# Kernel tuning notes

Hardware: AMD Instinct MI355X
Metric: run time of the kernel (lower is better)

Reference implementation:

```python
import jax, jax.numpy as jnp
import numpy as np

B, S, D, H = 2, 2048, 2048, 16
HD = D // H  # 128


def _rope_tables(seq_len, head_dim, base=10000.0):
    inv_freq = 1.0 / (base ** (np.arange(0, head_dim, 2, dtype=np.float32) / head_dim))
    t = np.arange(seq_len, dtype=np.float32)
    freqs = np.outer(t, inv_freq)  # [S, HD/2]
    return jnp.asarray(np.cos(freqs)), jnp.asarray(np.sin(freqs))


def setup_inputs() -> dict:
    key = jax.random.key(0)
    ks = jax.random.split(key, 5)
    std = 0.02
    inp = {
        "x": jax.random.normal(ks[0], (B, S, D), jnp.float32),
        "wq": jax.random.normal(ks[1], (D, D), jnp.float32) * std,
        "bq": jnp.zeros((D,), jnp.float32),
        "wk": jax.random.normal(ks[2], (D, D), jnp.float32) * std,
        "bk": jnp.zeros((D,), jnp.float32),
        "wv": jax.random.normal(ks[3], (D, D), jnp.float32) * std,
        "bv": jnp.zeros((D,), jnp.float32),
        "wo": jax.random.normal(ks[4], (D, D), jnp.float32) * std,
        "bo": jnp.zeros((D,), jnp.float32),
    }
    cos, sin = _rope_tables(S, HD)
    inp["freqs_cos"], inp["freqs_sin"] = cos, sin
    return inp


def _apply_rope(t, cos, sin):
    # t: [B,S,H,HD]; cos/sin: [S,HD/2] -> broadcast [1,S,1,HD/2]
    tp = t.reshape(*t.shape[:-1], HD // 2, 2)
    t1, t2 = tp[..., 0], tp[..., 1]
    c = cos[None, :, None, :]
    s = sin[None, :, None, :]
    out = jnp.stack([t1 * c - t2 * s, t1 * s + t2 * c], axis=-1)
    return out.reshape(t.shape)


def reference(x, wq, bq, wk, bk, wv, bv, wo, bo, freqs_cos, freqs_sin):
    b, s, d = x.shape
    q = (x @ wq.T + bq).reshape(b, s, H, HD)
    k = (x @ wk.T + bk).reshape(b, s, H, HD)
    v = (x @ wv.T + bv).reshape(b, s, H, HD)
    q = _apply_rope(q, freqs_cos, freqs_sin)
    k = _apply_rope(k, freqs_cos, freqs_sin)
    # causal SDPA: scores [B,H,S,S]
    scale = 1.0 / jnp.sqrt(jnp.asarray(HD, x.dtype))
    scores = jnp.einsum("bqhd,bkhd->bhqk", q, k) * scale
    causal = jnp.tril(jnp.ones((s, s), bool))
    scores = jnp.where(causal[None, None], scores, jnp.asarray(-1e30, scores.dtype))
    attn = jax.nn.softmax(scores.astype(jnp.float32), axis=-1).astype(x.dtype)
    out = jnp.einsum("bhqk,bkhd->bqhd", attn, v).reshape(b, s, d)
    return out @ wo.T + bo
```

## Files before the change

### kernel.cpp

```cpp
#include <hip/hip_runtime.h>


typedef __attribute__((ext_vector_type(8))) short short8;
typedef __attribute__((ext_vector_type(4))) float f32x4;
typedef __attribute__((ext_vector_type(16))) float f32x16;
typedef __attribute__((ext_vector_type(2))) unsigned short u16x2;
typedef __attribute__((ext_vector_type(4))) unsigned short u16x4;
typedef __attribute__((ext_vector_type(8))) unsigned short u16x8;

constexpr int Bc = 2, Sc = 2048, Dc = 2048, Hc = 16, HDc = 128;
constexpr int Mc = Bc * Sc;
constexpr int Nc = Dc, Kc = Dc;
constexpr float QSCL = 0.08838834764831845f * 1.4426950408889634f;

__device__ __forceinline__ unsigned short f2bf(float f) {
    union { float f; unsigned u; } x; x.f = f;
    unsigned r = x.u + 0x7FFFu + ((x.u >> 16) & 1u);
    return (unsigned short)(r >> 16);
}
__device__ __forceinline__ float bf2f(unsigned short u) {
    union { float f; unsigned u; } x; x.u = (unsigned)u << 16; return x.f;
}

__device__ __forceinline__ void g2lds16(const void* g, void* l) {
    __builtin_amdgcn_global_load_lds(
        (const __attribute__((address_space(1))) void*)g,
        (__attribute__((address_space(3))) void*)l, 16, 0, 0);
}

__device__ __forceinline__ void cvt_body(const float* __restrict__ in,
                                         unsigned short* __restrict__ out, int i) {
    f32x4 a = *((const f32x4*)in + (size_t)i * 2);
    f32x4 b = *((const f32x4*)in + (size_t)i * 2 + 1);
    u16x8 o;
    o[0] = f2bf(a[0]); o[1] = f2bf(a[1]); o[2] = f2bf(a[2]); o[3] = f2bf(a[3]);
    o[4] = f2bf(b[0]); o[5] = f2bf(b[1]); o[6] = f2bf(b[2]); o[7] = f2bf(b[3]);
    *((u16x8*)out + i) = o;
}

__global__ __launch_bounds__(256) void cvt_f32_bf16(
    const float* __restrict__ in, unsigned short* __restrict__ out, int n8) {
    int i = blockIdx.x * 256 + threadIdx.x;
    if (i >= n8) return;
    cvt_body(in, out, i);
}

__global__ __launch_bounds__(256) void cvt_batch(
    const float* __restrict__ x,  unsigned short* __restrict__ xo,
    const float* __restrict__ w0, unsigned short* __restrict__ o0,
    const float* __restrict__ w1, unsigned short* __restrict__ o1,
    const float* __restrict__ w2, unsigned short* __restrict__ o2,
    const float* __restrict__ w3, unsigned short* __restrict__ o3) {
    const int which = blockIdx.y;
    const float* in; unsigned short* out; int n8;
    if (which == 0)      { in = x;  out = xo; n8 = (Mc * Dc) / 8; }
    else if (which == 1) { in = w0; out = o0; n8 = (Dc * Dc) / 8; }
    else if (which == 2) { in = w1; out = o1; n8 = (Dc * Dc) / 8; }
    else if (which == 3) { in = w2; out = o2; n8 = (Dc * Dc) / 8; }
    else                 { in = w3; out = o3; n8 = (Dc * Dc) / 8; }
    int i = blockIdx.x * 256 + threadIdx.x;
    if (i >= n8) return;
    cvt_body(in, out, i);
}

template <int MODE>
__global__ __launch_bounds__(256) void gemm_nt(
    const unsigned short* __restrict__ A, const unsigned short* __restrict__ W,
    const float* __restrict__ bias, const float* __restrict__ rc,
    const float* __restrict__ rs, void* __restrict__ outp) {
    __shared__ __align__(16) unsigned short As[128 * 64];
    __shared__ __align__(16) unsigned short Bs[128 * 64];
    const int tid = threadIdx.x;
    const int w = tid >> 6, l = tid & 63;
    const int wm = w >> 1, wn = w & 1;
    const int lrow = l & 15, lhi = l >> 4;
    const int m0 = blockIdx.y * 128, n0 = blockIdx.x * 128;

    f32x4 acc[4][4];
#pragma unroll
    for (int i = 0; i < 4; ++i)
#pragma unroll
        for (int j = 0; j < 4; ++j) acc[i][j] = (f32x4){0.f, 0.f, 0.f, 0.f};

    for (int k0 = 0; k0 < Kc; k0 += 64) {
        __syncthreads();
#pragma unroll
        for (int i = 0; i < 4; ++i) {
            int s = i * 256 + tid;
            int row = s >> 3, c = s & 7;
            int cg = (c ^ (row & 7)) * 8;
            g2lds16(A + (size_t)(m0 + row) * Kc + k0 + cg,
                    &As[(size_t)(i * 256 + (w << 6)) * 8]);
            g2lds16(W + (size_t)(n0 + row) * Kc + k0 + cg,
                    &Bs[(size_t)(i * 256 + (w << 6)) * 8]);
        }
        __syncthreads();
#pragma unroll
        for (int kk = 0; kk < 2; ++kk) {
            short8 af[4], bf[4];
#pragma unroll
            for (int i = 0; i < 4; ++i) {
                int ra = wm * 64 + i * 16 + lrow;
                af[i] = *(const short8*)&As[ra * 64 + (((kk * 4 + lhi) ^ (ra & 7)) << 3)];
                int rb = wn * 64 + i * 16 + lrow;
                bf[i] = *(const short8*)&Bs[rb * 64 + (((kk * 4 + lhi) ^ (rb & 7)) << 3)];
            }
#pragma unroll
            for (int i = 0; i < 4; ++i)
#pragma unroll
                for (int j = 0; j < 4; ++j)
                    acc[i][j] = __builtin_amdgcn_mfma_f32_16x16x32_bf16(
                        af[i], bf[j], acc[i][j], 0, 0, 0);
        }
    }

#pragma unroll
    for (int i = 0; i < 4; ++i) {
#pragma unroll
        for (int j = 0; j < 4; ++j) {
            int gm0 = m0 + wm * 64 + i * 16 + lhi * 4;
            int gn  = n0 + wn * 64 + j * 16 + lrow;
            float bv = bias[gn];
            if (MODE == 0 || MODE == 1) {
                unsigned short* o = (unsigned short*)outp;
                int fi = (gn & (HDc - 1)) >> 1;
#pragma unroll
                for (int r = 0; r < 4; ++r) {
                    int gm = gm0 + r;
                    float v = acc[i][j][r] + bv;
                    float p = __shfl_xor(v, 1);
                    int pos = gm & (Sc - 1);
                    float cz = rc[pos * (HDc / 2) + fi];
                    float sz = rs[pos * (HDc / 2) + fi];
                    float ov = (gn & 1) ? (p * sz + v * cz) : (v * cz - p * sz);
                    if (MODE == 0) ov *= QSCL;
                    o[(size_t)gm * Nc + gn] = f2bf(ov);
                }
            } else if (MODE == 2) {
                unsigned short* o = (unsigned short*)outp;
                int b = gm0 >> 11, sb = gm0 & (Sc - 1);
                u16x4 pk;
#pragma unroll
                for (int r = 0; r < 4; ++r) pk[r] = f2bf(acc[i][j][r] + bv);
                *(u16x4*)&o[((size_t)b * Dc + gn) * Sc + sb] = pk;
            } else {
                float* o = (float*)outp;
#pragma unroll
                for (int r = 0; r < 4; ++r)
                    o[(size_t)(gm0 + r) * Nc + gn] = acc[i][j][r] + bv;
            }
        }
    }
}

#define ATTN_STAGE(tt, kd, vd) {                                               \
    const unsigned short* Kt = Kbase + (size_t)(tt) * 64 * Dc;                 \
    const unsigned short* Vp = Vbase + (tt) * 64;                              \
    _Pragma("unroll")                                                          \
    for (int i_ = 0; i_ < 4; ++i_) {                                           \
        int p_ = i_ * 256 + tid;                                               \
        int rK = p_ >> 4, sK = p_ & 15;                                        \
        g2lds16(Kt + (size_t)rK * Dc + ((sK ^ (rK & 15)) << 3),                \
                (kd) + (i_ * 256 + (w << 6)) * 8);                             \
        int rV = p_ >> 3, sV = p_ & 7;                                         \
        g2lds16(Vp + (size_t)rV * Sc + ((sV ^ (rV & 7)) << 3),                 \
                (vd) + (i_ * 256 + (w << 6)) * 8);                             \
    } }

#define ATTN_PVSTEP(PC, HB, KS) {                                              \
    int X0, X1, Y0, Y1;                                                        \
    asm("v_cvt_pk_bf16_f32 %0, %1, %2" : "=v"(X0) : "v"(PC[HB+0]), "v"(PC[HB+1])); \
    asm("v_cvt_pk_bf16_f32 %0, %1, %2" : "=v"(X1) : "v"(PC[HB+2]), "v"(PC[HB+3])); \
    asm("v_cvt_pk_bf16_f32 %0, %1, %2" : "=v"(Y0) : "v"(PC[HB+4]), "v"(PC[HB+5])); \
    asm("v_cvt_pk_bf16_f32 %0, %1, %2" : "=v"(Y1) : "v"(PC[HB+6]), "v"(PC[HB+7])); \
    asm("v_permlane32_swap_b32 %0, %1" : "+v"(X0), "+v"(Y0));                  \
    asm("v_permlane32_swap_b32 %0, %1" : "+v"(X1), "+v"(Y1));                  \
    union { int i[4]; short8 s; } pf_;                                         \
    pf_.i[0] = X0; pf_.i[1] = X1; pf_.i[2] = Y0; pf_.i[3] = Y1;                \
    _Pragma("unroll")                                                          \
    for (int dc_ = 0; dc_ < 4; ++dc_) {                                        \
        int rr = 32 * dc_ + ql;                                                \
        short8 vf = *(const short8*)&Vbuf[rr * 64 + (((2*(KS)+Hh) ^ (rr & 7)) << 3)]; \
        accv[dc_] = __builtin_amdgcn_mfma_f32_32x32x16_bf16(vf, pf_.s, accv[dc_], 0, 0, 0); \
    } }

#define ATTN_TILE_BODY(Kbuf, Vbuf, kb0)                                        \
    {                                                                          \
        f32x16 a0 = (f32x16)(0.f), a1 = (f32x16)(0.f);                         \
        __builtin_amdgcn_s_setprio(1);                                         \
        _Pragma("unroll")                                                      \
        for (int dc = 0; dc < 8; ++dc) {                                       \
            int r0 = ql, r1 = 32 + ql, sl = dc * 2 + Hh;                       \
            short8 k0 = *(const short8*)&Kbuf[r0 * 128 + ((sl ^ (r0 & 15)) << 3)]; \
            short8 k1 = *(const short8*)&Kbuf[r1 * 128 + ((sl ^ (r1 & 15)) << 3)]; \
            a0 = __builtin_amdgcn_mfma_f32_32x32x16_bf16(k0, qf[dc], a0, 0, 0, 0); \
            a1 = __builtin_amdgcn_mfma_f32_32x32x16_bf16(k1, qf[dc], a1, 0, 0, 0); \
        }                                                                      \
        __builtin_amdgcn_s_setprio(0);                                         \
        if ((kb0) >= 2 * qt * 64) {                                            \
            _Pragma("unroll")                                                  \
            for (int r = 0; r < 16; ++r) {                                     \
                int kl = (r & 3) + 8 * (r >> 2) + 4 * Hh;                      \
                if ((kb0) + kl > qg)      a0[r] = -3.0e38f;                    \
                if ((kb0) + 32 + kl > qg) a1[r] = -3.0e38f;                    \
            }                                                                  \
        }                                                                      \
        float m8[8];                                                           \
        _Pragma("unroll")                                                      \
        for (int r = 0; r < 8; ++r)                                            \
            m8[r] = fmaxf(fmaxf(a0[r], a0[r + 8]), fmaxf(a1[r], a1[r + 8]));   \
        float m4a = fmaxf(m8[0], m8[1]), m4b = fmaxf(m8[2], m8[3]);            \
        float m4c = fmaxf(m8[4], m8[5]), m4d = fmaxf(m8[6], m8[7]);            \
        float pm = fmaxf(fmaxf(m4a, m4b), fmaxf(m4c, m4d));                    \
        pm = fmaxf(pm, __shfl_xor(pm, 32));                                    \
        if (!__all(pm - mrun <= 8.0f)) {                                       \
            float mnew = fmaxf(mrun, pm);                                      \
            float fs = exp2f(mrun - mnew);                                     \
            mrun = mnew;                                                       \
            lrun *= fs;                                                        \
            _Pragma("unroll")                                                  \
            for (int dc = 0; dc < 4; ++dc)                                     \
                _Pragma("unroll")                                              \
                for (int r = 0; r < 16; ++r) accv[dc][r] *= fs;                \
        }                                                                      \
        float p0[16], p1[16];                                                  \
        _Pragma("unroll")                                                      \
        for (int r = 0; r < 16; ++r) p0[r] = exp2f(a0[r] - mrun);              \
        _Pragma("unroll")                                                      \
        for (int r = 0; r < 16; ++r) p1[r] = exp2f(a1[r] - mrun);              \
        float s8[8];                                                           \
        _Pragma("unroll")                                                      \
        for (int r = 0; r < 8; ++r)                                            \
            s8[r] = (p0[r] + p0[r + 8]) + (p1[r] + p1[r + 8]);                 \
        float s4a = s8[0] + s8[1], s4b = s8[2] + s8[3];                        \
        float s4c = s8[4] + s8[5], s4d = s8[6] + s8[7];                        \
        float ps = (s4a + s4b) + (s4c + s4d);                                  \
        lrun += ps + __shfl_xor(ps, 32);                                       \
        __builtin_amdgcn_s_setprio(1);                                         \
        ATTN_PVSTEP(p0, 0, 0); ATTN_PVSTEP(p0, 8, 1);                          \
        ATTN_PVSTEP(p1, 0, 2); ATTN_PVSTEP(p1, 8, 3);                          \
        __builtin_amdgcn_s_setprio(0);                                         \
    }

__global__ __launch_bounds__(256, 2) void attn_part(
    const unsigned short* __restrict__ Q, const unsigned short* __restrict__ Kb,
    const unsigned short* __restrict__ Vt, unsigned short* __restrict__ O,
    unsigned short* __restrict__ pacc, float* __restrict__ pml) {
    __shared__ __align__(16) unsigned short Ks[2][64 * 128];
    __shared__ __align__(16) unsigned short Vs[2][128 * 64];
    const int tid = threadIdx.x;
    const int w = tid >> 6, l = tid & 63;
    const int ql = l & 31, Hh = l >> 5;
    const int bh = blockIdx.x;
    const int slot = blockIdx.y;
    int qt, part, np;
    if (slot < 16) { qt = 15 - (slot >> 1); part = slot & 1; np = 2; }
    else           { qt = 23 - slot;        part = 0;        np = 1; }
    const int nt   = 2 * qt + 2;
    const int tbeg = part ? (qt + 1) : 0;
    const int tend = (np == 2 && part == 0) ? (qt + 1) : nt;
    const int b = bh >> 4, h = bh & 15;

    const unsigned short* Kbase = Kb + ((size_t)b * Sc) * Dc + h * HDc;
    const unsigned short* Vbase = Vt + ((size_t)b * Dc + h * HDc) * Sc;

    const int qw0 = qt * 128 + w * 32;
    const int qg = qw0 + ql;

    short8 qf[8];
    {
        const unsigned short* qp = Q + ((size_t)(b * Sc + qg)) * Dc + h * HDc;
#pragma unroll
        for (int dc = 0; dc < 8; ++dc)
            qf[dc] = *(const short8*)(qp + dc * 16 + Hh * 8);
    }
    f32x16 accv[4];
#pragma unroll
    for (int i = 0; i < 4; ++i) accv[i] = (f32x16)(0.f);
    float mrun = -3.0e38f, lrun = 0.f;

    ATTN_STAGE(tbeg, Ks[0], Vs[0]);
    for (int t = tbeg; t < tend; ++t) {
        const int cur = (t - tbeg) & 1;
        if (t + 1 < tend) {
            ATTN_STAGE(t + 1, Ks[cur ^ 1], Vs[cur ^ 1]);
            asm volatile("s_waitcnt vmcnt(8)" ::: "memory");
        } else {
            asm volatile("s_waitcnt vmcnt(0)" ::: "memory");
        }
        __builtin_amdgcn_s_barrier();

        const unsigned short* Kbuf = Ks[cur];
        const unsigned short* Vbuf = Vs[cur];
        const int kb0 = t * 64;
        if (kb0 <= qw0 + 31) ATTN_TILE_BODY(Kbuf, Vbuf, kb0);
        __builtin_amdgcn_s_barrier();
    }

    if (np == 1) {
        float inv = 1.f / lrun;
        unsigned short* Op = O + ((size_t)(b * Sc + qg)) * Dc + h * HDc;
#pragma unroll
        for (int dc = 0; dc < 4; ++dc)
#pragma unroll
            for (int rg = 0; rg < 4; ++rg) {
                int d0 = 32 * dc + 8 * rg + 4 * Hh;
                u16x4 pk;
#pragma unroll
                for (int j = 0; j < 4; ++j) pk[j] = f2bf(accv[dc][rg * 4 + j] * inv);
                *(u16x4*)(Op + d0) = pk;
            }
    } else {
        const int jslot = ((bh << 3) + (qt - 8)) * 2 + part;
        unsigned short* pa = pacc + (size_t)jslot * (128 * 128) + (w * 32 + ql) * 128;
#pragma unroll
        for (int dc = 0; dc < 4; ++dc)
#pragma unroll
            for (int rg = 0; rg < 4; ++rg) {
                u16x4 pk;
#pragma unroll
                for (int j = 0; j < 4; ++j) pk[j] = f2bf(accv[dc][rg * 4 + j]);
                *(u16x4*)&pa[32 * dc + 8 * rg + 4 * Hh] = pk;
            }
        if (Hh == 0) {
            float* pm2 = pml + (size_t)jslot * 256 + (w * 32 + ql) * 2;
            pm2[0] = mrun; pm2[1] = lrun;
        }
    }
}

__global__ __launch_bounds__(256) void attn_combine(
    const unsigned short* __restrict__ pacc, const float* __restrict__ pml,
    unsigned short* __restrict__ O) {
    const int w = threadIdx.x >> 6, l = threadIdx.x & 63;
    const int idx = blockIdx.x * 4 + w;
    const int jp = idx >> 7, row = idx & 127;
    const int bh = jp >> 3, qt = (jp & 7) + 8;
    const int b = bh >> 4, h = bh & 15;
    const unsigned short* a0 = pacc + ((size_t)jp * 2) * (128 * 128) + row * 128;
    const unsigned short* a1 = a0 + 128 * 128;
    const float* ml0 = pml + ((size_t)jp * 2) * 256 + row * 2;
    const float* ml1 = ml0 + 256;
    float m0 = ml0[0], l0 = ml0[1], m1 = ml1[0], l1 = ml1[1];
    float M = fmaxf(m0, m1);
    float w0 = exp2f(m0 - M), w1 = exp2f(m1 - M);
    float inv = 1.f / (l0 * w0 + l1 * w1);
    int d = l * 2;
    u16x2 v0 = *(const u16x2*)&a0[d];
    u16x2 v1 = *(const u16x2*)&a1[d];
    u16x2 pk;
    pk[0] = f2bf((bf2f(v0[0]) * w0 + bf2f(v1[0]) * w1) * inv);
    pk[1] = f2bf((bf2f(v0[1]) * w0 + bf2f(v1[1]) * w1) * inv);
    int qrow = qt * 128 + row;
    *(u16x2*)(O + ((size_t)(b * Sc + qrow)) * Dc + h * HDc + d) = pk;
}

__global__ __launch_bounds__(256, 2) void attn_fwd5(
    const unsigned short* __restrict__ Q, const unsigned short* __restrict__ Kb,
    const unsigned short* __restrict__ Vt, unsigned short* __restrict__ O) {
    __shared__ __align__(16) unsigned short Ks[2][64 * 128];
    __shared__ __align__(16) unsigned short Vs[2][128 * 64];
    const int tid = threadIdx.x;
    const int w = tid >> 6, l = tid & 63;
    const int ql = l & 31, Hh = l >> 5;
    const int bh = blockIdx.x;
    const int y = blockIdx.y;
    const int qt = (y < 8) ? y : (23 - y);
    const int b = bh >> 4, h = bh & 15;

    const unsigned short* Kbase = Kb + ((size_t)b * Sc) * Dc + h * HDc;
    const unsigned short* Vbase = Vt + ((size_t)b * Dc + h * HDc) * Sc;

    const int qw0 = qt * 128 + w * 32;
    const int qg = qw0 + ql;

    short8 qf[8];
    {
        const unsigned short* qp = Q + ((size_t)(b * Sc + qg)) * Dc + h * HDc;
#pragma unroll
        for (int dc = 0; dc < 8; ++dc)
            qf[dc] = *(const short8*)(qp + dc * 16 + Hh * 8);
    }
    f32x16 accv[4];
#pragma unroll
    for (int i = 0; i < 4; ++i) accv[i] = (f32x16)(0.f);
    float mrun = -3.0e38f, lrun = 0.f;
    const int nt = 2 * qt + 2;

    ATTN_STAGE(0, Ks[0], Vs[0]);
    for (int t = 0; t < nt; ++t) {
        if (t + 1 < nt) {
            ATTN_STAGE(t + 1, Ks[(t + 1) & 1], Vs[(t + 1) & 1]);
            asm volatile("s_waitcnt vmcnt(8)" ::: "memory");
        } else {
            asm volatile("s_waitcnt vmcnt(0)" ::: "memory");
        }
        __builtin_amdgcn_s_barrier();

        const unsigned short* Kbuf = Ks[t & 1];
        const unsigned short* Vbuf = Vs[t & 1];
        const int kb0 = t * 64;
        if (kb0 <= qw0 + 31) ATTN_TILE_BODY(Kbuf, Vbuf, kb0);
        __builtin_amdgcn_s_barrier();
    }
    float inv = 1.f / lrun;
    unsigned short* Op = O + ((size_t)(b * Sc + qg)) * Dc + h * HDc;
#pragma unroll
    for (int dc = 0; dc < 4; ++dc)
#pragma unroll
        for (int rg = 0; rg < 4; ++rg) {
            int d0 = 32 * dc + 8 * rg + 4 * Hh;
            u16x4 pk;
#pragma unroll
            for (int j = 0; j < 4; ++j) pk[j] = f2bf(accv[dc][rg * 4 + j] * inv);
            *(u16x4*)(Op + d0) = pk;
        }
}

extern "C" void kernel_launch(void* const* d_in, const int* in_sizes, int n_in,
                              void* d_out, int out_size, void* d_ws, size_t ws_size,
                              hipStream_t stream) {
    const float* x  = (const float*)d_in[0];
    const float* wq = (const float*)d_in[1];
    const float* bq = (const float*)d_in[2];
    const float* wk = (const float*)d_in[3];
    const float* bk = (const float*)d_in[4];
    const float* wv = (const float*)d_in[5];
    const float* bv = (const float*)d_in[6];
    const float* wo = (const float*)d_in[7];
    const float* bo = (const float*)d_in[8];
    const float* rc = (const float*)d_in[9];
    const float* rs = (const float*)d_in[10];

    const size_t NE = (size_t)Mc * Dc;
    const size_t NW = (size_t)Dc * Dc;

    unsigned short* xb = (unsigned short*)d_ws;
    unsigned short* qb = xb + NE;
    unsigned short* kb = qb + NE;
    unsigned short* vt = kb + NE;
    unsigned short* wb = vt + NE;

    const int ne8 = (int)(NE / 8), nw8 = (int)(NW / 8);
    dim3 gg(Nc / 128, Mc / 128), tb(256);
    const bool big_ws = ws_size >= (4 * NE + 4 * NW) * sizeof(unsigned short);

    if (big_ws) {
        unsigned short* wqb = wb;
        unsigned short* wkb = wb + NW;
        unsigned short* wvb = wb + 2 * NW;
        unsigned short* wob = wb + 3 * NW;
        unsigned short* pacc = wb;
        float* pml = (float*)(wb + 2 * NW);
        cvt_batch<<<dim3(ne8 / 256, 5), tb, 0, stream>>>(
            x, xb, wq, wqb, wk, wkb, wv, wvb, wo, wob);
        gemm_nt<0><<<gg, tb, 0, stream>>>(xb, wqb, bq, rc, rs, qb);
        gemm_nt<1><<<gg, tb, 0, stream>>>(xb, wkb, bk, rc, rs, kb);
        gemm_nt<2><<<gg, tb, 0, stream>>>(xb, wvb, bv, rc, rs, vt);
        attn_part<<<dim3(Bc * Hc, 24), tb, 0, stream>>>(qb, kb, vt, xb, pacc, pml);
        attn_combine<<<dim3(32 * 8 * 128 / 4), tb, 0, stream>>>(pacc, pml, xb);
        gemm_nt<3><<<gg, tb, 0, stream>>>(xb, wob, bo, rc, rs, d_out);
    } else {
        cvt_f32_bf16<<<dim3(ne8 / 256), tb, 0, stream>>>(x, xb, ne8);
        cvt_f32_bf16<<<dim3(nw8 / 256), tb, 0, stream>>>(wq, wb, nw8);
        gemm_nt<0><<<gg, tb, 0, stream>>>(xb, wb, bq, rc, rs, qb);
        cvt_f32_bf16<<<dim3(nw8 / 256), tb, 0, stream>>>(wk, wb, nw8);
        gemm_nt<1><<<gg, tb, 0, stream>>>(xb, wb, bk, rc, rs, kb);
        cvt_f32_bf16<<<dim3(nw8 / 256), tb, 0, stream>>>(wv, wb, nw8);
        gemm_nt<2><<<gg, tb, 0, stream>>>(xb, wb, bv, rc, rs, vt);
        attn_fwd5<<<dim3(Bc * Hc, 16), tb, 0, stream>>>(qb, kb, vt, xb);
        cvt_f32_bf16<<<dim3(nw8 / 256), tb, 0, stream>>>(wo, wb, nw8);
        gemm_nt<3><<<gg, tb, 0, stream>>>(xb, wb, bo, rc, rs, d_out);
    }
}
```

Measured before the change: 274.1 us.

## Fuse QKV projections into one triple-buffered 256x128 GEMM with 512 threads

Replaces the three separate Q/K/V GEMM launches with one gemm8 launch over the concatenated weight matrix (contiguous wq/wk/wv bf16 buffers), picking bias and epilogue (RoPE, transpose) per column block. The new kernel uses 256x128 tiles, 8 waves, a 3-stage LDS ring filled with global_load_lds, interleaved staging with MFMA, and setprio around MFMA bursts. The output projection also uses this kernel. It cuts launch count and improves overlap, at the cost of large LDS use (144KB per block) which limits occupancy.

```diff
diff --git a/kernel.cpp b/kernel.cpp
--- a/kernel.cpp
+++ b/kernel.cpp
@@ -11,6 +11,7 @@
 constexpr int Bc = 2, Sc = 2048, Dc = 2048, Hc = 16, HDc = 128;
 constexpr int Mc = Bc * Sc;
 constexpr int Nc = Dc, Kc = Dc;
+constexpr int NT = Kc / 64;
 constexpr float QSCL = 0.08838834764831845f * 1.4426950408889634f;
 
 __device__ __forceinline__ unsigned short f2bf(float f) {
@@ -61,6 +62,126 @@
     int i = blockIdx.x * 256 + threadIdx.x;
     if (i >= n8) return;
     cvt_body(in, out, i);
+}
+
+#define G8_STAGE_A(tt, rr, ii) {                                               \
+    int s_ = (ii) * 512 + tid, row_ = s_ >> 3, c_ = s_ & 7;                    \
+    g2lds16(A + (size_t)(m0 + row_) * Kc + (tt) * 64 + ((c_ ^ (row_ & 7)) << 3), \
+            &As[rr][(size_t)((ii) * 512 + (w << 6)) * 8]); }
+#define G8_STAGE_B(tt, rr, ii) {                                               \
+    int s_ = (ii) * 512 + tid, row_ = s_ >> 3, c_ = s_ & 7;                    \
+    g2lds16(W + (size_t)(n0 + row_) * Kc + (tt) * 64 + ((c_ ^ (row_ & 7)) << 3), \
+            &Bs[rr][(size_t)((ii) * 512 + (w << 6)) * 8]); }
+#define G8_RD_B(rr, kk) { _Pragma("unroll")                                    \
+    for (int j = 0; j < 4; ++j) {                                              \
+        int rb = wn * 64 + j * 16 + lrow;                                      \
+        bf[j] = *(const short8*)&Bs[rr][rb * 64 + ((((kk)*4 + lhi) ^ (rb & 7)) << 3)]; } }
+#define G8_RD_A(rr, kk, i0) {                                                  \
+    { int ra = wm * 64 + (i0) * 16 + lrow;                                     \
+      af0 = *(const short8*)&As[rr][ra * 64 + ((((kk)*4 + lhi) ^ (ra & 7)) << 3)]; } \
+    { int ra = wm * 64 + ((i0) + 1) * 16 + lrow;                               \
+      af1 = *(const short8*)&As[rr][ra * 64 + ((((kk)*4 + lhi) ^ (ra & 7)) << 3)]; } }
+#define G8_MFMA(i0) { _Pragma("unroll")                                        \
+    for (int j = 0; j < 4; ++j) {                                              \
+        acc[i0][j] = __builtin_amdgcn_mfma_f32_16x16x32_bf16(af0, bf[j], acc[i0][j], 0, 0, 0); \
+        acc[(i0)+1][j] = __builtin_amdgcn_mfma_f32_16x16x32_bf16(af1, bf[j], acc[(i0)+1][j], 0, 0, 0); } }
+#define G8_SYNC1 __builtin_amdgcn_s_barrier();                                 \
+    asm volatile("s_waitcnt lgkmcnt(0)" ::: "memory");                         \
+    __builtin_amdgcn_s_setprio(1);
+#define G8_SYNC2 __builtin_amdgcn_s_setprio(0); __builtin_amdgcn_s_barrier();
+
+template <int KIND>
+__global__ __launch_bounds__(512, 2) void gemm8(
+    const unsigned short* __restrict__ A, const unsigned short* __restrict__ W,
+    const float* __restrict__ bq, const float* __restrict__ bk,
+    const float* __restrict__ bv, const float* __restrict__ rc,
+    const float* __restrict__ rs, void* __restrict__ oq,
+    unsigned short* __restrict__ ok, unsigned short* __restrict__ ov) {
+    __shared__ __align__(16) unsigned short As[3][256 * 64];
+    __shared__ __align__(16) unsigned short Bs[3][128 * 64];
+    const int tid = threadIdx.x;
+    const int w = tid >> 6, l = tid & 63;
+    const int wm = w >> 1, wn = w & 1;
+    const int lrow = l & 15, lhi = l >> 4;
+    const int m0 = blockIdx.y * 256, n0 = blockIdx.x * 128;
+
+    f32x4 acc[4][4];
+#pragma unroll
+    for (int i = 0; i < 4; ++i)
+#pragma unroll
+        for (int j = 0; j < 4; ++j) acc[i][j] = (f32x4){0.f, 0.f, 0.f, 0.f};
+
+#pragma unroll
+    for (int ii = 0; ii < 4; ++ii) G8_STAGE_A(0, 0, ii);
+    G8_STAGE_B(0, 0, 0); G8_STAGE_B(0, 0, 1);
+#pragma unroll
+    for (int ii = 0; ii < 4; ++ii) G8_STAGE_A(1, 1, ii);
+    G8_STAGE_B(1, 1, 0); G8_STAGE_B(1, 1, 1);
+    asm volatile("s_waitcnt vmcnt(6)" ::: "memory");
+    __builtin_amdgcn_s_barrier();
+
+    short8 bf[4], af0, af1;
+    for (int t = 0; t < NT; ++t) {
+        const int r = t % 3, rn = (t + 2) % 3;
+        const bool st = (t + 2) < NT;
+        G8_RD_B(r, 0); G8_RD_A(r, 0, 0);
+        if (st) { G8_STAGE_A(t + 2, rn, 0); G8_STAGE_A(t + 2, rn, 1); }
+        G8_SYNC1; G8_MFMA(0); G8_SYNC2;
+        G8_RD_A(r, 0, 2);
+        if (st) { G8_STAGE_A(t + 2, rn, 2); G8_STAGE_A(t + 2, rn, 3); }
+        G8_SYNC1; G8_MFMA(2); G8_SYNC2;
+        G8_RD_B(r, 1); G8_RD_A(r, 1, 0);
+        if (st) G8_STAGE_B(t + 2, rn, 0);
+        G8_SYNC1; G8_MFMA(0); G8_SYNC2;
+        G8_RD_A(r, 1, 2);
+        if (st) {
+            G8_STAGE_B(t + 2, rn, 1);
+            asm volatile("s_waitcnt vmcnt(6)" ::: "memory");
+        } else {
+            asm volatile("s_waitcnt vmcnt(0)" ::: "memory");
+        }
+        G8_SYNC1; G8_MFMA(2); G8_SYNC2;
+    }
+
+    const int mode = (KIND == 1) ? 3 : (n0 >> 11);
+    const float* bias = (KIND == 1) ? bq : (mode == 0 ? bq : mode == 1 ? bk : bv);
+#pragma unroll
+    for (int i = 0; i < 4; ++i) {
+#pragma unroll
+        for (int j = 0; j < 4; ++j) {
+            int gm0 = m0 + wm * 64 + i * 16 + lhi * 4;
+            int gn  = n0 + wn * 64 + j * 16 + lrow;
+            int gnl = gn & (Dc - 1);
+            float bvv = bias[gnl];
+            if (mode == 0 || mode == 1) {
+                unsigned short* o = (unsigned short*)(mode == 0 ? oq : (void*)ok);
+                int fi = (gn & (HDc - 1)) >> 1;
+#pragma unroll
+                for (int rr = 0; rr < 4; ++rr) {
+                    int gm = gm0 + rr;
+                    float v = acc[i][j][rr] + bvv;
+                    float p = __shfl_xor(v, 1);
+                    int pos = gm & (Sc - 1);
+                    float cz = rc[pos * (HDc / 2) + fi];
+                    float sz = rs[pos * (HDc / 2) + fi];
+                    float ovv = (gn & 1) ? (p * sz + v * cz) : (v * cz - p * sz);
+                    if (mode == 0) ovv *= QSCL;
+                    o[(size_t)gm * Dc + gnl] = f2bf(ovv);
+                }
+            } else if (mode == 2) {
+                int b = gm0 >> 11, sb = gm0 & (Sc - 1);
+                u16x4 pk;
+#pragma unroll
+                for (int rr = 0; rr < 4; ++rr) pk[rr] = f2bf(acc[i][j][rr] + bvv);
+                *(u16x4*)&ov[((size_t)b * Dc + gnl) * Sc + sb] = pk;
+            } else {
+                float* o = (float*)oq;
+#pragma unroll
+                for (int rr = 0; rr < 4; ++rr)
+                    o[(size_t)(gm0 + rr) * Nc + gn] = acc[i][j][rr] + bvv;
+            }
+        }
+    }
 }
 
 template <int MODE>
@@ -442,7 +563,7 @@
     unsigned short* wb = vt + NE;
 
     const int ne8 = (int)(NE / 8), nw8 = (int)(NW / 8);
-    dim3 gg(Nc / 128, Mc / 128), tb(256);
+    dim3 tb(256);
     const bool big_ws = ws_size >= (4 * NE + 4 * NW) * sizeof(unsigned short);
 
     if (big_ws) {
@@ -454,13 +575,14 @@
         float* pml = (float*)(wb + 2 * NW);
         cvt_batch<<<dim3(ne8 / 256, 5), tb, 0, stream>>>(
             x, xb, wq, wqb, wk, wkb, wv, wvb, wo, wob);
-        gemm_nt<0><<<gg, tb, 0, stream>>>(xb, wqb, bq, rc, rs, qb);
-        gemm_nt<1><<<gg, tb, 0, stream>>>(xb, wkb, bk, rc, rs, kb);
-        gemm_nt<2><<<gg, tb, 0, stream>>>(xb, wvb, bv, rc, rs, vt);
+        gemm8<0><<<dim3(Nc * 3 / 128, Mc / 256), dim3(512), 0, stream>>>(
+            xb, wb, bq, bk, bv, rc, rs, qb, kb, vt);
         attn_part<<<dim3(Bc * Hc, 24), tb, 0, stream>>>(qb, kb, vt, xb, pacc, pml);
         attn_combine<<<dim3(32 * 8 * 128 / 4), tb, 0, stream>>>(pacc, pml, xb);
-        gemm_nt<3><<<gg, tb, 0, stream>>>(xb, wob, bo, rc, rs, d_out);
+        gemm8<1><<<dim3(Nc / 128, Mc / 256), dim3(512), 0, stream>>>(
+            xb, wob, bo, nullptr, nullptr, rc, rs, d_out, nullptr, nullptr);
     } else {
+        dim3 gg(Nc / 128, Mc / 128);
         cvt_f32_bf16<<<dim3(ne8 / 256), tb, 0, stream>>>(x, xb, ne8);
         cvt_f32_bf16<<<dim3(nw8 / 256), tb, 0, stream>>>(wq, wb, nw8);
         gemm_nt<0><<<gg, tb, 0, stream>>>(xb, wb, bq, rc, rs, qb);
```

New measurement: 293.8 us. +7.2%, slower.
